# Kernel tuning notes

Hardware: AMD Instinct MI355X
Metric: run time of the kernel (lower is better)

The kernel has to match this reference:

```python
import jax, jax.numpy as jnp
import numpy as np

BINS = 64
EPS = 1e-8


def _compute_histogram(gray, bins=BINS):
    # gray: [B, H, W] -> normalized histogram [B, bins]
    B = gray.shape[0]
    flat = gray.reshape(B, -1)                      # [B, N]
    mn = flat.min(axis=1, keepdims=True)
    mx = flat.max(axis=1, keepdims=True)
    valid = mx > mn                                  # [B, 1]
    norm = (flat - mn) / jnp.where(valid, mx - mn, 1.0)
    idx = jnp.clip((norm * (bins - 1)).astype(jnp.int32), 0, bins - 1)  # [B, N]
    # per-image bincount via scatter-add
    hist = jax.vmap(lambda i: jnp.zeros(bins, dtype=flat.dtype).at[i].add(1.0))(idx)
    hist = hist / hist.sum(axis=1, keepdims=True)
    return jnp.where(valid, hist, jnp.full_like(hist, 1.0 / bins))


def reference(x, y, lambda_cc=10.0):
    # channel balance
    x_mean = jnp.mean(x, axis=(2, 3), keepdims=True)   # [B,3,1,1]
    y_mean = jnp.mean(y, axis=(2, 3), keepdims=True)
    x_bal = x_mean / (jnp.sum(x_mean, axis=1, keepdims=True) + EPS)
    y_bal = y_mean / (jnp.sum(y_mean, axis=1, keepdims=True) + EPS)
    color_balance_loss = jnp.mean(jnp.abs(x_bal - y_bal))

    # luminance
    x_gray = 0.299 * x[:, 0] + 0.587 * x[:, 1] + 0.114 * x[:, 2]  # [B,H,W]
    y_gray = 0.299 * y[:, 0] + 0.587 * y[:, 1] + 0.114 * y[:, 2]

    x_hist = _compute_histogram(x_gray)
    y_hist = _compute_histogram(y_gray)

    # F.kl_div(log(x_hist+eps), y_hist, reduction='batchmean')
    log_in = jnp.log(x_hist + EPS)
    ylogy = jnp.where(y_hist > 0, y_hist * jnp.log(jnp.where(y_hist > 0, y_hist, 1.0)), 0.0)
    kl = jnp.sum(ylogy - y_hist * log_in) / x.shape[0]

    return lambda_cc * (color_balance_loss + kl)


def setup_inputs() -> dict:
    key = jax.random.key(0)
    k1, k2 = jax.random.split(key)
    x = jax.random.uniform(k1, (16, 3, 512, 512), dtype=jnp.float32)
    y = jax.random.uniform(k2, (16, 3, 512, 512), dtype=jnp.float32)
    return {"x": x, "y": y}
```

## Files before the change

kernel.cpp:

```cpp
#include <hip/hip_runtime.h>

#define HW_N (512 * 512)
#define BINS 64
#define BPI 64
#define TPB 256

struct ImgStats {
    double sumx[3];
    double sumy[3];
    unsigned int minx, maxx, miny, maxy;
    unsigned int histx[BINS];
    unsigned int histy[BINS];
};

__device__ __forceinline__ unsigned int f2ord(float f) {
    unsigned int u = __float_as_uint(f);
    return (u & 0x80000000u) ? ~u : (u | 0x80000000u);
}
__device__ __forceinline__ float ord2f(unsigned int u) {
    u = (u & 0x80000000u) ? (u ^ 0x80000000u) : ~u;
    return __uint_as_float(u);
}

__device__ __forceinline__ float grayf(float r, float g, float b) {
    return 0.299f * r + 0.587f * g + 0.114f * b;
}

__device__ __forceinline__ double waveSumD(double v) {
#pragma unroll
    for (int o = 32; o > 0; o >>= 1) v += __shfl_down(v, o);
    return v;
}
__device__ __forceinline__ float waveMinF(float v) {
#pragma unroll
    for (int o = 32; o > 0; o >>= 1) v = fminf(v, __shfl_down(v, o));
    return v;
}
__device__ __forceinline__ float waveMaxF(float v) {
#pragma unroll
    for (int o = 32; o > 0; o >>= 1) v = fmaxf(v, __shfl_down(v, o));
    return v;
}

__global__ void k_init(ImgStats* st, int B) {
    const int nwords = B * (int)(sizeof(ImgStats) / 4);
    unsigned int* w = (unsigned int*)st;
    for (int i = threadIdx.x; i < nwords; i += blockDim.x) w[i] = 0u;
    __syncthreads();
    for (int i = threadIdx.x; i < B * 2; i += blockDim.x) {
        int b = i >> 1;
        if (i & 1) st[b].miny = 0xFFFFFFFFu;
        else       st[b].minx = 0xFFFFFFFFu;
    }
}

__global__ __launch_bounds__(TPB) void k_reduce(const float* __restrict__ x,
                                                const float* __restrict__ y,
                                                ImgStats* __restrict__ st) {
    const int b   = blockIdx.x / BPI;
    const int sub = blockIdx.x % BPI;
    const int qPerBlock = (HW_N / 4) / BPI;
    const int q0 = sub * qPerBlock;
    const size_t base = (size_t)b * 3 * HW_N;

    const float4* xr = (const float4*)(x + base);
    const float4* xg = (const float4*)(x + base + HW_N);
    const float4* xb = (const float4*)(x + base + 2 * HW_N);
    const float4* yr = (const float4*)(y + base);
    const float4* yg = (const float4*)(y + base + HW_N);
    const float4* yb = (const float4*)(y + base + 2 * HW_N);

    float s0 = 0.f, s1 = 0.f, s2 = 0.f;
    float t0 = 0.f, t1 = 0.f, t2 = 0.f;
    float mnx = 3.4e38f, mxx = -3.4e38f;
    float mny = 3.4e38f, mxy = -3.4e38f;

    for (int i = threadIdx.x; i < qPerBlock; i += TPB) {
        const int q = q0 + i;
        float4 r = xr[q], g = xg[q], bl = xb[q];
        s0 += (r.x + r.y) + (r.z + r.w);
        s1 += (g.x + g.y) + (g.z + g.w);
        s2 += (bl.x + bl.y) + (bl.z + bl.w);
        {
            float g0 = grayf(r.x, g.x, bl.x), g1 = grayf(r.y, g.y, bl.y);
            float g2 = grayf(r.z, g.z, bl.z), g3 = grayf(r.w, g.w, bl.w);
            mnx = fminf(mnx, fminf(fminf(g0, g1), fminf(g2, g3)));
            mxx = fmaxf(mxx, fmaxf(fmaxf(g0, g1), fmaxf(g2, g3)));
        }
        r = yr[q]; g = yg[q]; bl = yb[q];
        t0 += (r.x + r.y) + (r.z + r.w);
        t1 += (g.x + g.y) + (g.z + g.w);
        t2 += (bl.x + bl.y) + (bl.z + bl.w);
        {
            float g0 = grayf(r.x, g.x, bl.x), g1 = grayf(r.y, g.y, bl.y);
            float g2 = grayf(r.z, g.z, bl.z), g3 = grayf(r.w, g.w, bl.w);
            mny = fminf(mny, fminf(fminf(g0, g1), fminf(g2, g3)));
            mxy = fmaxf(mxy, fmaxf(fmaxf(g0, g1), fmaxf(g2, g3)));
        }
    }

    const int wave = threadIdx.x >> 6;
    const int lane = threadIdx.x & 63;
    __shared__ double shs[6][TPB / 64];
    __shared__ float  shmn[2][TPB / 64];
    __shared__ float  shmx[2][TPB / 64];

    double d;
    d = waveSumD((double)s0); if (!lane) shs[0][wave] = d;
    d = waveSumD((double)s1); if (!lane) shs[1][wave] = d;
    d = waveSumD((double)s2); if (!lane) shs[2][wave] = d;
    d = waveSumD((double)t0); if (!lane) shs[3][wave] = d;
    d = waveSumD((double)t1); if (!lane) shs[4][wave] = d;
    d = waveSumD((double)t2); if (!lane) shs[5][wave] = d;
    float f;
    f = waveMinF(mnx); if (!lane) shmn[0][wave] = f;
    f = waveMinF(mny); if (!lane) shmn[1][wave] = f;
    f = waveMaxF(mxx); if (!lane) shmx[0][wave] = f;
    f = waveMaxF(mxy); if (!lane) shmx[1][wave] = f;
    __syncthreads();

    if (threadIdx.x == 0) {
        atomicAdd(&st[b].sumx[0], shs[0][0] + shs[0][1] + shs[0][2] + shs[0][3]);
        atomicAdd(&st[b].sumx[1], shs[1][0] + shs[1][1] + shs[1][2] + shs[1][3]);
        atomicAdd(&st[b].sumx[2], shs[2][0] + shs[2][1] + shs[2][2] + shs[2][3]);
        atomicAdd(&st[b].sumy[0], shs[3][0] + shs[3][1] + shs[3][2] + shs[3][3]);
        atomicAdd(&st[b].sumy[1], shs[4][0] + shs[4][1] + shs[4][2] + shs[4][3]);
        atomicAdd(&st[b].sumy[2], shs[5][0] + shs[5][1] + shs[5][2] + shs[5][3]);
        float a;
        a = fminf(fminf(shmn[0][0], shmn[0][1]), fminf(shmn[0][2], shmn[0][3]));
        atomicMin(&st[b].minx, f2ord(a));
        a = fminf(fminf(shmn[1][0], shmn[1][1]), fminf(shmn[1][2], shmn[1][3]));
        atomicMin(&st[b].miny, f2ord(a));
        a = fmaxf(fmaxf(shmx[0][0], shmx[0][1]), fmaxf(shmx[0][2], shmx[0][3]));
        atomicMax(&st[b].maxx, f2ord(a));
        a = fmaxf(fmaxf(shmx[1][0], shmx[1][1]), fmaxf(shmx[1][2], shmx[1][3]));
        atomicMax(&st[b].maxy, f2ord(a));
    }
}

__global__ __launch_bounds__(TPB) void k_hist(const float* __restrict__ x,
                                              const float* __restrict__ y,
                                              ImgStats* __restrict__ st) {
    __shared__ unsigned int lh[8][BINS];
    for (int i = threadIdx.x; i < 8 * BINS; i += TPB) ((unsigned int*)lh)[i] = 0u;

    const int b   = blockIdx.x / BPI;
    const int sub = blockIdx.x % BPI;

    const float mnx = ord2f(st[b].minx), mxx = ord2f(st[b].maxx);
    const float mny = ord2f(st[b].miny), mxy = ord2f(st[b].maxy);
    const float rgx = (mxx > mnx) ? (mxx - mnx) : 1.0f;
    const float rgy = (mxy > mny) ? (mxy - mny) : 1.0f;
    __syncthreads();

    const int qPerBlock = (HW_N / 4) / BPI;
    const int q0 = sub * qPerBlock;
    const size_t base = (size_t)b * 3 * HW_N;

    const float4* xr = (const float4*)(x + base);
    const float4* xg = (const float4*)(x + base + HW_N);
    const float4* xb = (const float4*)(x + base + 2 * HW_N);
    const float4* yr = (const float4*)(y + base);
    const float4* yg = (const float4*)(y + base + HW_N);
    const float4* yb = (const float4*)(y + base + 2 * HW_N);

    const int wave = threadIdx.x >> 6;
    unsigned int* hx = lh[wave];
    unsigned int* hy = lh[4 + wave];

    for (int i = threadIdx.x; i < qPerBlock; i += TPB) {
        const int q = q0 + i;
        float4 r = xr[q], g = xg[q], bl = xb[q];
        {
            float gv[4] = { grayf(r.x, g.x, bl.x), grayf(r.y, g.y, bl.y),
                            grayf(r.z, g.z, bl.z), grayf(r.w, g.w, bl.w) };
#pragma unroll
            for (int j = 0; j < 4; j++) {
                float t = ((gv[j] - mnx) / rgx) * 63.0f;
                int id = (int)t;
                id = id < 0 ? 0 : (id > 63 ? 63 : id);
                atomicAdd(&hx[id], 1u);
            }
        }
        r = yr[q]; g = yg[q]; bl = yb[q];
        {
            float gv[4] = { grayf(r.x, g.x, bl.x), grayf(r.y, g.y, bl.y),
                            grayf(r.z, g.z, bl.z), grayf(r.w, g.w, bl.w) };
#pragma unroll
            for (int j = 0; j < 4; j++) {
                float t = ((gv[j] - mny) / rgy) * 63.0f;
                int id = (int)t;
                id = id < 0 ? 0 : (id > 63 ? 63 : id);
                atomicAdd(&hy[id], 1u);
            }
        }
    }
    __syncthreads();

    for (int i = threadIdx.x; i < 2 * BINS; i += TPB) {
        const int src = i >> 6, bin = i & 63;
        unsigned int v = lh[src * 4 + 0][bin] + lh[src * 4 + 1][bin] +
                         lh[src * 4 + 2][bin] + lh[src * 4 + 3][bin];
        if (v) atomicAdd(src ? &st[b].histy[bin] : &st[b].histx[bin], v);
    }
}

__global__ __launch_bounds__(1024) void k_final(const ImgStats* __restrict__ st,
                                                float* __restrict__ out, int B) {
    const int tid = threadIdx.x;
    double klt = 0.0, cbt = 0.0;

    for (int t = tid; t < B * BINS; t += 1024) {
        const int b = t >> 6, bin = t & 63;
        const ImgStats& s = st[b];
        const float mnx = ord2f(s.minx), mxx = ord2f(s.maxx);
        const float mny = ord2f(s.miny), mxy = ord2f(s.maxy);
        const float invN = 1.0f / (float)HW_N;
        const float xh = (mxx > mnx) ? (float)s.histx[bin] * invN : (1.0f / BINS);
        const float yh = (mxy > mny) ? (float)s.histy[bin] * invN : (1.0f / BINS);
        const float log_in = logf(xh + 1e-8f);
        const float ylogy = (yh > 0.0f) ? yh * logf(yh) : 0.0f;
        klt += (double)ylogy - (double)yh * (double)log_in;
    }

    for (int t = tid; t < B * 3; t += 1024) {
        const int b = t / 3, c = t % 3;
        const ImgStats& s = st[b];
        const double N = (double)HW_N;
        const double xb = (s.sumx[c] / N) /
                          ((s.sumx[0] + s.sumx[1] + s.sumx[2]) / N + 1e-8);
        const double yb = (s.sumy[c] / N) /
                          ((s.sumy[0] + s.sumy[1] + s.sumy[2]) / N + 1e-8);
        cbt += fabs(xb - yb);
    }

    __shared__ double skl[16], scb[16];
    const double kw = waveSumD(klt);
    const double cw = waveSumD(cbt);
    const int wave = tid >> 6, lane = tid & 63;
    if (!lane) { skl[wave] = kw; scb[wave] = cw; }
    __syncthreads();
    if (tid == 0) {
        double K = 0.0, C = 0.0;
        for (int i = 0; i < 16; i++) { K += skl[i]; C += scb[i]; }
        const double kl = K / (double)B;
        const double cb = C / (double)(B * 3);
        out[0] = (float)(10.0 * (cb + kl));
    }
}

extern "C" void kernel_launch(void* const* d_in, const int* in_sizes, int n_in,
                              void* d_out, int out_size, void* d_ws, size_t ws_size,
                              hipStream_t stream) {
    const float* x = (const float*)d_in[0];
    const float* y = (const float*)d_in[1];
    float* out = (float*)d_out;
    const int B = in_sizes[0] / (3 * HW_N);

    ImgStats* st = (ImgStats*)d_ws;

    k_init<<<1, 256, 0, stream>>>(st, B);
    k_reduce<<<B * BPI, TPB, 0, stream>>>(x, y, st);
    k_hist<<<B * BPI, TPB, 0, stream>>>(x, y, st);
    k_final<<<1, 1024, 0, stream>>>(st, out, B);
}
```

Before: 140.3 us.

## Merge init and final kernels into two passes with per-block partials

Drops the separate init and final launches. The first pass now writes per-block partial sums and min/max to workspace instead of doing global atomics, and zeroes the histograms and counter itself. The second pass reduces the per-image min/max across those partials with wave shuffles, and the last block to finish, found through an atomic counter, computes the final loss. This saves two kernel launches and the atomic contention on the stats, at the cost of a serial tail in one block and reliance on threadfence ordering.

```diff
diff --git a/kernel.cpp b/kernel.cpp
--- a/kernel.cpp
+++ b/kernel.cpp
@@ -2,25 +2,21 @@
 
 #define HW_N (512 * 512)
 #define BINS 64
-#define BPI 64
-#define TPB 256
-
-struct ImgStats {
-    double sumx[3];
-    double sumy[3];
-    unsigned int minx, maxx, miny, maxy;
-    unsigned int histx[BINS];
-    unsigned int histy[BINS];
+#define BPI  64
+#define TPB  256
+#define QPB  ((HW_N / 4) / BPI)
+#define MAXB 16
+
+struct Part {
+    double sum[6];
+    float  mn[2];
+    float  mx[2];
 };
 
 __device__ __forceinline__ unsigned int f2ord(float f) {
     unsigned int u = __float_as_uint(f);
     return (u & 0x80000000u) ? ~u : (u | 0x80000000u);
 }
-__device__ __forceinline__ float ord2f(unsigned int u) {
-    u = (u & 0x80000000u) ? (u ^ 0x80000000u) : ~u;
-    return __uint_as_float(u);
-}
 
 __device__ __forceinline__ float grayf(float r, float g, float b) {
     return 0.299f * r + 0.587f * g + 0.114f * b;
@@ -31,36 +27,32 @@
     for (int o = 32; o > 0; o >>= 1) v += __shfl_down(v, o);
     return v;
 }
-__device__ __forceinline__ float waveMinF(float v) {
-#pragma unroll
-    for (int o = 32; o > 0; o >>= 1) v = fminf(v, __shfl_down(v, o));
+__device__ __forceinline__ float waveMinAll(float v) {
+#pragma unroll
+    for (int o = 32; o > 0; o >>= 1) v = fminf(v, __shfl_xor(v, o));
     return v;
 }
-__device__ __forceinline__ float waveMaxF(float v) {
-#pragma unroll
-    for (int o = 32; o > 0; o >>= 1) v = fmaxf(v, __shfl_down(v, o));
+__device__ __forceinline__ float waveMaxAll(float v) {
+#pragma unroll
+    for (int o = 32; o > 0; o >>= 1) v = fmaxf(v, __shfl_xor(v, o));
     return v;
 }
 
-__global__ void k_init(ImgStats* st, int B) {
-    const int nwords = B * (int)(sizeof(ImgStats) / 4);
-    unsigned int* w = (unsigned int*)st;
-    for (int i = threadIdx.x; i < nwords; i += blockDim.x) w[i] = 0u;
-    __syncthreads();
-    for (int i = threadIdx.x; i < B * 2; i += blockDim.x) {
-        int b = i >> 1;
-        if (i & 1) st[b].miny = 0xFFFFFFFFu;
-        else       st[b].minx = 0xFFFFFFFFu;
-    }
-}
-
-__global__ __launch_bounds__(TPB) void k_reduce(const float* __restrict__ x,
-                                                const float* __restrict__ y,
-                                                ImgStats* __restrict__ st) {
-    const int b   = blockIdx.x / BPI;
-    const int sub = blockIdx.x % BPI;
-    const int qPerBlock = (HW_N / 4) / BPI;
-    const int q0 = sub * qPerBlock;
+__global__ __launch_bounds__(TPB) void k_pass1(const float* __restrict__ x,
+                                               const float* __restrict__ y,
+                                               Part* __restrict__ part,
+                                               unsigned int* __restrict__ img_hist,
+                                               unsigned int* __restrict__ counter) {
+    const int tid = threadIdx.x;
+    const int blk = blockIdx.x;
+    const int b   = blk / BPI;
+    const int sub = blk % BPI;
+
+    if (sub == 0)
+        for (int i = tid; i < 2 * BINS; i += TPB) img_hist[b * 2 * BINS + i] = 0u;
+    if (blk == 0 && tid == 0) *counter = 0u;
+
+    const int q0 = sub * QPB;
     const size_t base = (size_t)b * 3 * HW_N;
 
     const float4* xr = (const float4*)(x + base);
@@ -75,7 +67,7 @@
     float mnx = 3.4e38f, mxx = -3.4e38f;
     float mny = 3.4e38f, mxy = -3.4e38f;
 
-    for (int i = threadIdx.x; i < qPerBlock; i += TPB) {
+    for (int i = tid; i < QPB; i += TPB) {
         const int q = q0 + i;
         float4 r = xr[q], g = xg[q], bl = xb[q];
         s0 += (r.x + r.y) + (r.z + r.w);
@@ -99,8 +91,8 @@
         }
     }
 
-    const int wave = threadIdx.x >> 6;
-    const int lane = threadIdx.x & 63;
+    const int wave = tid >> 6;
+    const int lane = tid & 63;
     __shared__ double shs[6][TPB / 64];
     __shared__ float  shmn[2][TPB / 64];
     __shared__ float  shmx[2][TPB / 64];
@@ -113,50 +105,54 @@
     d = waveSumD((double)t1); if (!lane) shs[4][wave] = d;
     d = waveSumD((double)t2); if (!lane) shs[5][wave] = d;
     float f;
-    f = waveMinF(mnx); if (!lane) shmn[0][wave] = f;
-    f = waveMinF(mny); if (!lane) shmn[1][wave] = f;
-    f = waveMaxF(mxx); if (!lane) shmx[0][wave] = f;
-    f = waveMaxF(mxy); if (!lane) shmx[1][wave] = f;
-    __syncthreads();
-
-    if (threadIdx.x == 0) {
-        atomicAdd(&st[b].sumx[0], shs[0][0] + shs[0][1] + shs[0][2] + shs[0][3]);
-        atomicAdd(&st[b].sumx[1], shs[1][0] + shs[1][1] + shs[1][2] + shs[1][3]);
-        atomicAdd(&st[b].sumx[2], shs[2][0] + shs[2][1] + shs[2][2] + shs[2][3]);
-        atomicAdd(&st[b].sumy[0], shs[3][0] + shs[3][1] + shs[3][2] + shs[3][3]);
-        atomicAdd(&st[b].sumy[1], shs[4][0] + shs[4][1] + shs[4][2] + shs[4][3]);
-        atomicAdd(&st[b].sumy[2], shs[5][0] + shs[5][1] + shs[5][2] + shs[5][3]);
-        float a;
-        a = fminf(fminf(shmn[0][0], shmn[0][1]), fminf(shmn[0][2], shmn[0][3]));
-        atomicMin(&st[b].minx, f2ord(a));
-        a = fminf(fminf(shmn[1][0], shmn[1][1]), fminf(shmn[1][2], shmn[1][3]));
-        atomicMin(&st[b].miny, f2ord(a));
-        a = fmaxf(fmaxf(shmx[0][0], shmx[0][1]), fmaxf(shmx[0][2], shmx[0][3]));
-        atomicMax(&st[b].maxx, f2ord(a));
-        a = fmaxf(fmaxf(shmx[1][0], shmx[1][1]), fmaxf(shmx[1][2], shmx[1][3]));
-        atomicMax(&st[b].maxy, f2ord(a));
-    }
-}
-
-__global__ __launch_bounds__(TPB) void k_hist(const float* __restrict__ x,
-                                              const float* __restrict__ y,
-                                              ImgStats* __restrict__ st) {
+    f = waveMinAll(mnx); if (!lane) shmn[0][wave] = f;
+    f = waveMinAll(mny); if (!lane) shmn[1][wave] = f;
+    f = waveMaxAll(mxx); if (!lane) shmx[0][wave] = f;
+    f = waveMaxAll(mxy); if (!lane) shmx[1][wave] = f;
+    __syncthreads();
+
+    if (tid == 0) {
+        Part& p = part[blk];
+        p.sum[0] = shs[0][0] + shs[0][1] + shs[0][2] + shs[0][3];
+        p.sum[1] = shs[1][0] + shs[1][1] + shs[1][2] + shs[1][3];
+        p.sum[2] = shs[2][0] + shs[2][1] + shs[2][2] + shs[2][3];
+        p.sum[3] = shs[3][0] + shs[3][1] + shs[3][2] + shs[3][3];
+        p.sum[4] = shs[4][0] + shs[4][1] + shs[4][2] + shs[4][3];
+        p.sum[5] = shs[5][0] + shs[5][1] + shs[5][2] + shs[5][3];
+        p.mn[0] = fminf(fminf(shmn[0][0], shmn[0][1]), fminf(shmn[0][2], shmn[0][3]));
+        p.mn[1] = fminf(fminf(shmn[1][0], shmn[1][1]), fminf(shmn[1][2], shmn[1][3]));
+        p.mx[0] = fmaxf(fmaxf(shmx[0][0], shmx[0][1]), fmaxf(shmx[0][2], shmx[0][3]));
+        p.mx[1] = fmaxf(fmaxf(shmx[1][0], shmx[1][1]), fmaxf(shmx[1][2], shmx[1][3]));
+    }
+}
+
+__global__ __launch_bounds__(TPB) void k_pass2(const float* __restrict__ x,
+                                               const float* __restrict__ y,
+                                               const Part* __restrict__ part,
+                                               unsigned int* __restrict__ img_hist,
+                                               unsigned int* __restrict__ counter,
+                                               float* __restrict__ out, int B) {
+    const int tid = threadIdx.x;
+    const int blk = blockIdx.x;
+    const int b   = blk / BPI;
+    const int sub = blk % BPI;
+    const int wave = tid >> 6;
+    const int lane = tid & 63;
+
+    const float4 mm = *(const float4*)&part[b * BPI + lane].mn[0];
+    const float imnx = waveMinAll(mm.x);
+    const float imny = waveMinAll(mm.y);
+    const float imxx = waveMaxAll(mm.z);
+    const float imxy = waveMaxAll(mm.w);
+    const float rgx = (imxx > imnx) ? (imxx - imnx) : 1.0f;
+    const float rgy = (imxy > imny) ? (imxy - imny) : 1.0f;
+
     __shared__ unsigned int lh[8][BINS];
-    for (int i = threadIdx.x; i < 8 * BINS; i += TPB) ((unsigned int*)lh)[i] = 0u;
-
-    const int b   = blockIdx.x / BPI;
-    const int sub = blockIdx.x % BPI;
-
-    const float mnx = ord2f(st[b].minx), mxx = ord2f(st[b].maxx);
-    const float mny = ord2f(st[b].miny), mxy = ord2f(st[b].maxy);
-    const float rgx = (mxx > mnx) ? (mxx - mnx) : 1.0f;
-    const float rgy = (mxy > mny) ? (mxy - mny) : 1.0f;
-    __syncthreads();
-
-    const int qPerBlock = (HW_N / 4) / BPI;
-    const int q0 = sub * qPerBlock;
+    for (int i = tid; i < 8 * BINS; i += TPB) ((unsigned int*)lh)[i] = 0u;
+    __syncthreads();
+
+    const int q0 = sub * QPB;
     const size_t base = (size_t)b * 3 * HW_N;
-
     const float4* xr = (const float4*)(x + base);
     const float4* xg = (const float4*)(x + base + HW_N);
     const float4* xb = (const float4*)(x + base + 2 * HW_N);
@@ -164,11 +160,10 @@
     const float4* yg = (const float4*)(y + base + HW_N);
     const float4* yb = (const float4*)(y + base + 2 * HW_N);
 
-    const int wave = threadIdx.x >> 6;
     unsigned int* hx = lh[wave];
     unsigned int* hy = lh[4 + wave];
 
-    for (int i = threadIdx.x; i < qPerBlock; i += TPB) {
+    for (int i = tid; i < QPB; i += TPB) {
         const int q = q0 + i;
         float4 r = xr[q], g = xg[q], bl = xb[q];
         {
@@ -176,7 +171,7 @@
                             grayf(r.z, g.z, bl.z), grayf(r.w, g.w, bl.w) };
 #pragma unroll
             for (int j = 0; j < 4; j++) {
-                float t = ((gv[j] - mnx) / rgx) * 63.0f;
+                float t = ((gv[j] - imnx) / rgx) * 63.0f;
                 int id = (int)t;
                 id = id < 0 ? 0 : (id > 63 ? 63 : id);
                 atomicAdd(&hx[id], 1u);
@@ -188,7 +183,7 @@
                             grayf(r.z, g.z, bl.z), grayf(r.w, g.w, bl.w) };
 #pragma unroll
             for (int j = 0; j < 4; j++) {
-                float t = ((gv[j] - mny) / rgy) * 63.0f;
+                float t = ((gv[j] - imny) / rgy) * 63.0f;
                 int id = (int)t;
                 id = id < 0 ? 0 : (id > 63 ? 63 : id);
                 atomicAdd(&hy[id], 1u);
@@ -197,52 +192,80 @@
     }
     __syncthreads();
 
-    for (int i = threadIdx.x; i < 2 * BINS; i += TPB) {
+    for (int i = tid; i < 2 * BINS; i += TPB) {
         const int src = i >> 6, bin = i & 63;
         unsigned int v = lh[src * 4 + 0][bin] + lh[src * 4 + 1][bin] +
                          lh[src * 4 + 2][bin] + lh[src * 4 + 3][bin];
-        if (v) atomicAdd(src ? &st[b].histy[bin] : &st[b].histx[bin], v);
-    }
-}
-
-__global__ __launch_bounds__(1024) void k_final(const ImgStats* __restrict__ st,
-                                                float* __restrict__ out, int B) {
-    const int tid = threadIdx.x;
+        if (v) atomicAdd(&img_hist[(b * 2 + src) * BINS + bin], v);
+    }
+
+    __threadfence();
+    __shared__ unsigned int s_last;
+    if (tid == 0) {
+        unsigned int old = atomicAdd(counter, 1u);
+        s_last = (old == gridDim.x - 1) ? 1u : 0u;
+    }
+    __syncthreads();
+    if (!s_last) return;
+    __threadfence();
+
+    __shared__ double ssum[MAXB][6];
+    __shared__ unsigned int somn[MAXB][2], somx[MAXB][2];
+    __shared__ double skl[TPB / 64], scb[TPB / 64];
+
+    for (int t = tid; t < B * 6; t += TPB) {
+        const int bb = t / 6, k = t - bb * 6;
+        double a = 0.0;
+#pragma unroll 8
+        for (int s = 0; s < BPI; s++) a += part[bb * BPI + s].sum[k];
+        ssum[bb][k] = a;
+    }
+    for (int t = tid; t < MAXB * 2; t += TPB) {
+        somn[t >> 1][t & 1] = 0xFFFFFFFFu;
+        somx[t >> 1][t & 1] = 0u;
+    }
+    __syncthreads();
+    for (int t = tid; t < B * BPI; t += TPB) {
+        const int bb = t >> 6, s = t & 63;
+        const Part& p = part[bb * BPI + s];
+        atomicMin(&somn[bb][0], f2ord(p.mn[0]));
+        atomicMin(&somn[bb][1], f2ord(p.mn[1]));
+        atomicMax(&somx[bb][0], f2ord(p.mx[0]));
+        atomicMax(&somx[bb][1], f2ord(p.mx[1]));
+    }
+    __syncthreads();
+
+    const float invN = 1.0f / (float)HW_N;
     double klt = 0.0, cbt = 0.0;
 
-    for (int t = tid; t < B * BINS; t += 1024) {
-        const int b = t >> 6, bin = t & 63;
-        const ImgStats& s = st[b];
-        const float mnx = ord2f(s.minx), mxx = ord2f(s.maxx);
-        const float mny = ord2f(s.miny), mxy = ord2f(s.maxy);
-        const float invN = 1.0f / (float)HW_N;
-        const float xh = (mxx > mnx) ? (float)s.histx[bin] * invN : (1.0f / BINS);
-        const float yh = (mxy > mny) ? (float)s.histy[bin] * invN : (1.0f / BINS);
+    for (int t = tid; t < B * BINS; t += TPB) {
+        const int bb = t >> 6, bin = t & 63;
+        const bool vldx = somx[bb][0] > somn[bb][0];
+        const bool vldy = somx[bb][1] > somn[bb][1];
+        const float xh = vldx ? (float)img_hist[(bb * 2 + 0) * BINS + bin] * invN : (1.0f / BINS);
+        const float yh = vldy ? (float)img_hist[(bb * 2 + 1) * BINS + bin] * invN : (1.0f / BINS);
         const float log_in = logf(xh + 1e-8f);
         const float ylogy = (yh > 0.0f) ? yh * logf(yh) : 0.0f;
         klt += (double)ylogy - (double)yh * (double)log_in;
     }
 
-    for (int t = tid; t < B * 3; t += 1024) {
-        const int b = t / 3, c = t % 3;
-        const ImgStats& s = st[b];
+    for (int t = tid; t < B * 3; t += TPB) {
+        const int bb = t / 3, c = t - bb * 3;
         const double N = (double)HW_N;
-        const double xb = (s.sumx[c] / N) /
-                          ((s.sumx[0] + s.sumx[1] + s.sumx[2]) / N + 1e-8);
-        const double yb = (s.sumy[c] / N) /
-                          ((s.sumy[0] + s.sumy[1] + s.sumy[2]) / N + 1e-8);
-        cbt += fabs(xb - yb);
-    }
-
-    __shared__ double skl[16], scb[16];
+        const double xbal = (ssum[bb][c] / N) /
+                            ((ssum[bb][0] + ssum[bb][1] + ssum[bb][2]) / N + 1e-8);
+        const double ybal = (ssum[bb][3 + c] / N) /
+                            ((ssum[bb][3] + ssum[bb][4] + ssum[bb][5]) / N + 1e-8);
+        cbt += fabs(xbal - ybal);
+    }
+
     const double kw = waveSumD(klt);
     const double cw = waveSumD(cbt);
-    const int wave = tid >> 6, lane = tid & 63;
     if (!lane) { skl[wave] = kw; scb[wave] = cw; }
     __syncthreads();
     if (tid == 0) {
         double K = 0.0, C = 0.0;
-        for (int i = 0; i < 16; i++) { K += skl[i]; C += scb[i]; }
+        for (int i = 0; i < TPB / 64; i++) { K += skl[i]; C += scb[i]; }
         const double kl = K / (double)B;
         const double cb = C / (double)(B * 3);
         out[0] = (float)(10.0 * (cb + kl));
@@ -257,10 +280,11 @@
     float* out = (float*)d_out;
     const int B = in_sizes[0] / (3 * HW_N);
 
-    ImgStats* st = (ImgStats*)d_ws;
-
-    k_init<<<1, 256, 0, stream>>>(st, B);
-    k_reduce<<<B * BPI, TPB, 0, stream>>>(x, y, st);
-    k_hist<<<B * BPI, TPB, 0, stream>>>(x, y, st);
-    k_final<<<1, 1024, 0, stream>>>(st, out, B);
-}
+    Part* part = (Part*)d_ws;
+    unsigned int* img_hist =
+        (unsigned int*)((char*)d_ws + (size_t)B * BPI * sizeof(Part));
+    unsigned int* counter = img_hist + B * 2 * BINS;
+
+    k_pass1<<<B * BPI, TPB, 0, stream>>>(x, y, part, img_hist, counter);
+    k_pass2<<<B * BPI, TPB, 0, stream>>>(x, y, part, img_hist, counter, out, B);
+}
```

Result: slower. 226.9 us (+61.7%).
